# Kernel optimization log

Hardware: AMD Instinct MI355X
Metric: run time of the kernel (lower is better)

## Reference

```python
import jax, jax.numpy as jnp
import numpy as np
from jax import lax

B, IN_CH, SKIP_CH, EMBED, H, W = 4, 256, 64, 64, 64, 64
RED = 8
QC = IN_CH // RED          # 32 q/k/v channels
GUIDE = 16.0
LN_EPS = 1e-5


def conv2d(x, w, b=None, groups=1):
    # x: [B,C,H,W], w: [O, C//groups, kh, kw], SAME padding, stride 1
    y = lax.conv_general_dilated(x, w, (1, 1), 'SAME',
                                 dimension_numbers=('NCHW', 'OIHW', 'NCHW'),
                                 feature_group_count=groups)
    return y if b is None else y + b[None, :, None, None]


def deform_conv(x, off, w, b):
    # torchvision DeformConv2d (DCNv1), 3x3, stride 1, pad 1
    # x: [B,C,H,W], off: [B,18,H,W] with (dy,dx) interleaved per kernel tap
    Bx, C, Hh, Ww = x.shape
    K = 9
    off = off.reshape(Bx, K, 2, Hh, Ww)
    gy, gx = jnp.meshgrid(jnp.arange(Hh, dtype=x.dtype),
                          jnp.arange(Ww, dtype=x.dtype), indexing='ij')
    kdy, kdx = jnp.meshgrid(jnp.arange(3, dtype=x.dtype) - 1,
                            jnp.arange(3, dtype=x.dtype) - 1, indexing='ij')
    py = gy[None, None] + kdy.reshape(K)[None, :, None, None] + off[:, :, 0]  # [B,K,H,W]
    px = gx[None, None] + kdx.reshape(K)[None, :, None, None] + off[:, :, 1]
    y0f = jnp.floor(py); x0f = jnp.floor(px)
    wy = py - y0f; wx = px - x0f
    y0 = y0f.astype(jnp.int32); x0 = x0f.astype(jnp.int32)

    def corner(yi, xi, wgt):
        valid = ((yi >= 0) & (yi < Hh) & (xi >= 0) & (xi < Ww)).astype(x.dtype)
        yc = jnp.clip(yi, 0, Hh - 1); xc = jnp.clip(xi, 0, Ww - 1)
        # per-batch gather -> [B, C, K, H, W]
        g = jax.vmap(lambda img, yy, xx: img[:, yy, xx])(x, yc, xc)
        return g * (wgt * valid)[:, None]

    vals = (corner(y0, x0, (1 - wy) * (1 - wx)) +
            corner(y0, x0 + 1, (1 - wy) * wx) +
            corner(y0 + 1, x0, wy * (1 - wx)) +
            corner(y0 + 1, x0 + 1, wy * wx))
    O = w.shape[0]
    return jnp.einsum('bckhw,ock->bohw', vals, w.reshape(O, C, K)) + b[None, :, None, None]


def setup_inputs() -> dict:
    key = jax.random.key(0)
    ks = jax.random.split(key, 16)
    rn = lambda k, s, sc=0.05: jax.random.normal(k, s, jnp.float32) * sc
    return {
        'x': jax.random.normal(ks[0], (B, IN_CH, H, W), jnp.float32),
        'skip': jax.random.normal(ks[1], (B, SKIP_CH, H // 2, W // 2), jnp.float32),
        'qkv_w': rn(ks[2], (3 * QC, IN_CH, 1, 1)), 'qkv_b': jnp.zeros((3 * QC,), jnp.float32),
        'proj_w': rn(ks[3], (IN_CH, QC, 1, 1)), 'proj_b': jnp.zeros((IN_CH,), jnp.float32),
        'edge_w': rn(ks[4], (SKIP_CH, 1, 3, 3)),
        'thick_w': rn(ks[5], (1, SKIP_CH, 1, 1)), 'thick_b': jnp.zeros((1,), jnp.float32),
        'off_w': rn(ks[6], (18, SKIP_CH, 3, 3), 0.02), 'off_b': jnp.zeros((18,), jnp.float32),
        'deform_w': rn(ks[7], (SKIP_CH, SKIP_CH, 3, 3)), 'deform_b': jnp.zeros((SKIP_CH,), jnp.float32),
        'ln_g': jnp.ones((EMBED,), jnp.float32), 'ln_b': jnp.zeros((EMBED,), jnp.float32),
        'mlp1_w': rn(ks[8], (4 * EMBED, EMBED, 1, 1)), 'mlp1_b': jnp.zeros((4 * EMBED,), jnp.float32),
        'dw_w': rn(ks[9], (4 * EMBED, 1, 3, 3)), 'dw_b': jnp.zeros((4 * EMBED,), jnp.float32),
        'mlp2_w': rn(ks[10], (EMBED, 4 * EMBED, 1, 1)), 'mlp2_b': jnp.zeros((EMBED,), jnp.float32),
        'down_w': rn(ks[11], (EMBED, IN_CH + SKIP_CH, 1, 1)), 'down_b': jnp.zeros((EMBED,), jnp.float32),
        'up_w': rn(ks[12], (IN_CH, EMBED, 1, 1)), 'up_b': jnp.zeros((IN_CH,), jnp.float32),
    }


def reference(x, skip, qkv_w, qkv_b, proj_w, proj_b, edge_w, thick_w, thick_b,
              off_w, off_b, deform_w, deform_b, ln_g, ln_b,
              mlp1_w, mlp1_b, dw_w, dw_b, mlp2_w, mlp2_b,
              down_w, down_b, up_w, up_b):
    Bx, C, Hh, Ww = x.shape
    # bilinear upsample (align_corners=False == half-pixel)
    skip_u = jax.image.resize(skip, (Bx, skip.shape[1], Hh, Ww), method='bilinear')

    # ---- EfficientCrossModalAttention ----
    qkv = conv2d(x, qkv_w, qkv_b)
    q, k, v = jnp.split(qkv, 3, axis=1)           # each [B, QC, H, W]
    c = q.shape[1]
    qf = q.reshape(Bx, c, Hh * Ww).transpose(0, 2, 1)   # [B, N, c]
    kf = k.reshape(Bx, c, Hh * Ww)                       # [B, c, N]
    vf = v.reshape(Bx, c, Hh * Ww).transpose(0, 2, 1)   # [B, N, c]
    attn = jax.nn.softmax(jnp.einsum('bnc,bcm->bnm', qf, kf) / jnp.sqrt(jnp.float32(c)), axis=-1)
    av = jnp.einsum('bnm,bmc->bnc', attn, vf).transpose(0, 2, 1).reshape(Bx, c, Hh, Ww)
    x2 = conv2d(av, proj_w, proj_b) + x

    # ---- edge / offset / deformable conv ----
    edge = conv2d(skip_u.mean(1, keepdims=True), edge_w)          # no bias
    thick = jax.nn.sigmoid(conv2d(skip_u, thick_w, thick_b))
    off = conv2d(edge, off_w, off_b) * (1.0 + GUIDE * thick)
    d = deform_conv(skip_u, off, deform_w, deform_b) + edge

    # ---- down -> TokenMixerBlock -> up ----
    e = conv2d(jnp.concatenate([x2, d], axis=1), down_w, down_b)  # [B, EMBED, H, W]
    h = e.transpose(0, 2, 3, 1)
    mu = h.mean(-1, keepdims=True)
    var = ((h - mu) ** 2).mean(-1, keepdims=True)
    h = (h - mu) / jnp.sqrt(var + LN_EPS) * ln_g + ln_b
    h = h.transpose(0, 3, 1, 2)
    h = jax.nn.gelu(conv2d(h, mlp1_w, mlp1_b), approximate=False)
    h = jax.nn.gelu(conv2d(h, dw_w, dw_b, groups=4 * EMBED), approximate=False)
    h = conv2d(h, mlp2_w, mlp2_b)
    t = h + e
    return conv2d(t, up_w, up_b)
```

## Files before the change

kernel.cpp:

```cpp
#include <hip/hip_runtime.h>
#include <hip/hip_bf16.h>
#include <math.h>

#define NB 4
#define NHW 4096
#define NBN (NB * NHW)

typedef const float* fp;
typedef unsigned short us;
typedef __attribute__((ext_vector_type(8))) short short8;
typedef __attribute__((ext_vector_type(4))) float floatx4;

__device__ __forceinline__ float b2f(__hip_bfloat16 v) { return __bfloat162float(v); }
__device__ __forceinline__ __hip_bfloat16 f2b(float v) { return __float2bfloat16(v); }
__device__ __forceinline__ us f2bu(float f) {
  __hip_bfloat16 h = __float2bfloat16(f);
  return *reinterpret_cast<us*>(&h);
}
__device__ __forceinline__ float bu2f(us u) {
  __hip_bfloat16 h = *reinterpret_cast<__hip_bfloat16*>(&u);
  return __bfloat162float(h);
}
__device__ __forceinline__ float gelu_ex(float x) { return 0.5f * x * (1.0f + erff(x * 0.70710678118654752f)); }
__device__ __forceinline__ short8 ld8(const us* p) { return *(const short8*)p; }

__global__ __launch_bounds__(256) void k_wq(fp qw, us* wq) {
  int i = blockIdx.x * 256 + threadIdx.x;
  if (i >= 96 * 256) return;
  wq[i] = f2bu(qw[i]);
}

__global__ __launch_bounds__(256) void k_wcast(fp pw, fp m1w, fp dnw, fp m2w, fp uw, fp dww,
                                               fp ew, fp ow, us* wc) {
  int i = blockIdx.x * 256 + threadIdx.x;
  if (i >= 99136) return;
  float v;
  if (i < 8192) v = pw[i];
  else if (i < 24576) v = m1w[i - 8192];
  else if (i < 45056) v = dnw[i - 24576];
  else if (i < 61440) v = m2w[i - 45056];
  else if (i < 77824) v = uw[i - 61440];
  else if (i < 80128) {
    int i2 = i - 77824;
    v = dww[(i2 & 255) * 9 + (i2 >> 8)];
  } else if (i < 80704) {
    int i2 = i - 80128;
    v = ew[(i2 & 63) * 9 + (i2 >> 6)];
  } else {
    int i2 = i - 80704;
    int oc = i2 / 576, rem = i2 % 576;
    int tap = rem >> 6, c = rem & 63;
    v = (oc < 18) ? ow[(oc * 64 + c) * 9 + tap] : 0.f;
  }
  wc[i] = f2bu(v);
}

__global__ __launch_bounds__(256) void k_wprep(fp dw, us* wbf) {
  int idx = blockIdx.x * 256 + threadIdx.x;
  if (idx >= 9 * 64 * 64) return;
  int c = idx & 63, oc = (idx >> 6) & 63, k = idx >> 12;
  wbf[idx] = f2bu(dw[(oc * 64 + c) * 9 + k]);
}

__global__ __launch_bounds__(256) void k_upsample(fp skip, float* su) {
  int idx = blockIdx.x * 256 + threadIdx.x;
  if (idx >= NB * 64 * NHW) return;
  int hw = idx & 4095, bc = idx >> 12;
  int y = hw >> 6, x = hw & 63;
  float fy = 0.5f * y - 0.25f, fx = 0.5f * x - 0.25f;
  float y0f = floorf(fy), x0f = floorf(fx);
  float wy = fy - y0f, wx = fx - x0f;
  int y0 = (int)y0f, x0 = (int)x0f;
  int y0c = min(31, max(0, y0)), y1c = min(31, max(0, y0 + 1));
  int x0c = min(31, max(0, x0)), x1c = min(31, max(0, x0 + 1));
  const float* p = skip + (size_t)bc * 1024;
  float v00 = p[y0c * 32 + x0c], v01 = p[y0c * 32 + x1c];
  float v10 = p[y1c * 32 + x0c], v11 = p[y1c * 32 + x1c];
  su[idx] = (1.f - wy) * ((1.f - wx) * v00 + wx * v01) + wy * ((1.f - wx) * v10 + wx * v11);
}

__global__ __launch_bounds__(256) void k_xpose(fp x, us* xT) {
  __shared__ float tile[64][65];
  int bid = blockIdx.x;
  int pt = bid & 63, ct = (bid >> 6) & 3, b = bid >> 8;
  int px0 = pt * 64, c0 = ct * 64;
  int tx = threadIdx.x & 63, ty = threadIdx.x >> 6;
  const float* src = x + ((size_t)(b * 256 + c0)) * NHW + px0;
#pragma unroll
  for (int i = 0; i < 16; i++) {
    int r = i * 4 + ty;
    tile[r][tx] = src[(size_t)r * NHW + tx];
  }
  __syncthreads();
  int cseg = threadIdx.x & 7, p0 = threadIdx.x >> 3;
#pragma unroll
  for (int h = 0; h < 2; h++) {
    int p = p0 + h * 32;
    short8 v;
#pragma unroll
    for (int j = 0; j < 8; j++) v[j] = (short)f2bu(tile[cseg * 8 + j][p]);
    *(short8*)&xT[((size_t)(b * NHW) + px0 + p) * 256 + c0 + cseg * 8] = v;
  }
}

__global__ __launch_bounds__(256) void k_qkv_g(const us* xT, const us* wq, fp bias, us* qkvb) {
  int wave = threadIdx.x >> 6, lane = threadIdx.x & 63;
  int quad = lane >> 4, l16 = lane & 15;
  int pxg0 = blockIdx.x * 64 + wave * 16;
  int b = pxg0 >> 12, hw0 = pxg0 & 4095;
  floatx4 acc[6];
#pragma unroll
  for (int m = 0; m < 6; m++) acc[m] = (floatx4){0.f, 0.f, 0.f, 0.f};
  const us* xrow = xT + (size_t)(pxg0 + l16) * 256 + quad * 8;
#pragma unroll
  for (int k0 = 0; k0 < 256; k0 += 32) {
    short8 bf = ld8(xrow + k0);
#pragma unroll
    for (int m = 0; m < 6; m++) {
      short8 af = ld8(wq + (size_t)(m * 16 + l16) * 256 + k0 + quad * 8);
      acc[m] = __builtin_amdgcn_mfma_f32_16x16x32_bf16(af, bf, acc[m], 0, 0, 0);
    }
  }
#pragma unroll
  for (int m = 0; m < 6; m++)
#pragma unroll
    for (int r = 0; r < 4; r++) {
      int oc = m * 16 + quad * 4 + r;
      float v = acc[m][r] + bias[oc];
      if (oc < 32) v *= 0.17677669529663688f;
      qkvb[(size_t)(b * 96 + oc) * NHW + hw0 + l16] = f2bu(v);
    }
}

__global__ __launch_bounds__(256) void k_attn(const us* qkvb, us* Opart, float* ml) {
  __shared__ __align__(16) us kt[128 * 40];
  __shared__ __align__(16) us vt[32 * 136];
  __shared__ __align__(16) us pt[4][16 * 136];
  int tid = threadIdx.x;
  int wave = tid >> 6, lane = tid & 63;
  int quad = lane >> 4, l16 = lane & 15;
  int blk = blockIdx.x;
  int kh = blk & 3;
  int rest = blk >> 2;
  int b = rest >> 6;
  int qbase = (rest & 63) * 64 + wave * 16;
  const us* qp = qkvb + (size_t)b * 96 * NHW;
  const us* kp = qp + 32 * NHW;
  const us* vp = qp + 64 * NHW;

  short8 aq;
#pragma unroll
  for (int j = 0; j < 8; j++)
    aq[j] = (short)qp[(size_t)(quad * 8 + j) * NHW + qbase + l16];

  float m_r[4], l_r[4];
  floatx4 o0 = {0.f, 0.f, 0.f, 0.f}, o1 = {0.f, 0.f, 0.f, 0.f};
#pragma unroll
  for (int r = 0; r < 4; r++) { m_r[r] = -1e30f; l_r[r] = 0.f; }

  int sc = tid & 31, sg = tid >> 5;
  int vc = tid >> 3, vs = tid & 7;

  int kb0 = kh * 1024;
  for (int kb = kb0; kb < kb0 + 1024; kb += 128) {
    __syncthreads();
    {
      const us* src = kp + (size_t)sc * NHW + kb + sg * 16;
#pragma unroll
      for (int j = 0; j < 16; j++) kt[(sg * 16 + j) * 40 + sc] = src[j];
      const us* sv = vp + (size_t)vc * NHW + kb + vs * 16;
      uint4 d0 = *(const uint4*)sv;
      uint4 d1 = *(const uint4*)(sv + 8);
      *(uint4*)&vt[vc * 136 + vs * 16] = d0;
      *(uint4*)&vt[vc * 136 + vs * 16 + 8] = d1;
    }
    __syncthreads();

    floatx4 s[8];
#pragma unroll
    for (int t = 0; t < 8; t++) {
      short8 bk = *(const short8*)&kt[(t * 16 + l16) * 40 + quad * 8];
      floatx4 z = {0.f, 0.f, 0.f, 0.f};
      s[t] = __builtin_amdgcn_mfma_f32_16x16x32_bf16(aq, bk, z, 0, 0, 0);
    }

    float mnew[4], alpha[4];
#pragma unroll
    for (int r = 0; r < 4; r++) {
      float mx = s[0][r];
#pragma unroll
      for (int t = 1; t < 8; t++) mx = fmaxf(mx, s[t][r]);
#pragma unroll
      for (int msk = 1; msk < 16; msk <<= 1) mx = fmaxf(mx, __shfl_xor(mx, msk, 64));
      mnew[r] = fmaxf(m_r[r], mx);
      alpha[r] = __expf(m_r[r] - mnew[r]);
      m_r[r] = mnew[r];
    }
    float rs[4] = {0.f, 0.f, 0.f, 0.f};
#pragma unroll
    for (int t = 0; t < 8; t++) {
#pragma unroll
      for (int r = 0; r < 4; r++) {
        float p = __expf(s[t][r] - mnew[r]);
        rs[r] += p;
        pt[wave][(quad * 4 + r) * 136 + t * 16 + l16] = f2bu(p);
      }
    }
#pragma unroll
    for (int r = 0; r < 4; r++) {
      float sm = rs[r];
#pragma unroll
      for (int msk = 1; msk < 16; msk <<= 1) sm += __shfl_xor(sm, msk, 64);
      l_r[r] = l_r[r] * alpha[r] + sm;
      o0[r] *= alpha[r];
      o1[r] *= alpha[r];
    }

#pragma unroll
    for (int t = 0; t < 4; t++) {
      short8 ap  = *(const short8*)&pt[wave][l16 * 136 + t * 32 + quad * 8];
      short8 bv0 = *(const short8*)&vt[l16 * 136 + t * 32 + quad * 8];
      short8 bv1 = *(const short8*)&vt[(l16 + 16) * 136 + t * 32 + quad * 8];
      o0 = __builtin_amdgcn_mfma_f32_16x16x32_bf16(ap, bv0, o0, 0, 0, 0);
      o1 = __builtin_amdgcn_mfma_f32_16x16x32_bf16(ap, bv1, o1, 0, 0, 0);
    }
  }

#pragma unroll
  for (int r = 0; r < 4; r++) {
    int q = qbase + quad * 4 + r;
    int qg = b * NHW + q;
    us* dst = Opart + ((size_t)(kh * NBN) + qg) * 32;
    dst[l16] = f2bu(o0[r]);
    dst[l16 + 16] = f2bu(o1[r]);
    if (l16 == 0) {
      ml[kh * NBN + qg] = m_r[r];
      ml[4 * NBN + kh * NBN + qg] = l_r[r];
    }
  }
}

__global__ __launch_bounds__(256) void k_merge(const us* Opart, const float* ml, us* avb) {
  int idx = blockIdx.x * 256 + threadIdx.x;
  int ch = idx & 31, qg = idx >> 5;
  float mk[4];
  float m = -1e30f;
#pragma unroll
  for (int kh = 0; kh < 4; kh++) { mk[kh] = ml[kh * NBN + qg]; m = fmaxf(m, mk[kh]); }
  float l = 0.f, v = 0.f;
#pragma unroll
  for (int kh = 0; kh < 4; kh++) {
    float a = __expf(mk[kh] - m);
    l += ml[4 * NBN + kh * NBN + qg] * a;
    v += bu2f(Opart[((size_t)(kh * NBN) + qg) * 32 + ch]) * a;
  }
  avb[idx] = f2bu(v / l);
}

__global__ __launch_bounds__(256) void k_proj_g(const us* avb, const us* xT, const us* wpj, fp bias, us* x2T) {
  int wave = threadIdx.x >> 6, lane = threadIdx.x & 63;
  int quad = lane >> 4, l16 = lane & 15;
  int pxg0 = blockIdx.x * 64 + wave * 16;
  short8 act = ld8(avb + (size_t)(pxg0 + l16) * 32 + quad * 8);
  floatx4 acc[16];
#pragma unroll
  for (int n = 0; n < 16; n++) {
    short8 wf = ld8(wpj + (size_t)(n * 16 + l16) * 32 + quad * 8);
    floatx4 z = {0.f, 0.f, 0.f, 0.f};
    acc[n] = __builtin_amdgcn_mfma_f32_16x16x32_bf16(act, wf, z, 0, 0, 0);
  }
#pragma unroll
  for (int n = 0; n < 16; n++)
#pragma unroll
    for (int r = 0; r < 4; r++) {
      int px = pxg0 + quad * 4 + r;
      int oc = n * 16 + l16;
      size_t oidx = (size_t)px * 256 + oc;
      x2T[oidx] = f2bu(acc[n][r] + bias[oc] + bu2f(xT[oidx]));
    }
}

__global__ __launch_bounds__(256) void k_meanthick(const float* su, fp tw, fp tb, float* sm, float* thick) {
  int idx = blockIdx.x * 256 + threadIdx.x;
  if (idx >= NB * NHW) return;
  int hw = idx & 4095, b = idx >> 12;
  const float* p = su + (size_t)b * 64 * NHW + hw;
  float s = 0.f, ts = 0.f;
#pragma unroll 8
  for (int c = 0; c < 64; c++) {
    float v = p[(size_t)c * NHW];
    s += v;
    ts += v * tw[c];
  }
  sm[idx] = s * (1.f / 64.f);
  float z = ts + tb[0];
  thick[idx] = 1.f / (1.f + __expf(-z));
}

__global__ __launch_bounds__(256) void k_edge_px(const float* sm, const us* ewT, us* edgeT) {
  int idx = blockIdx.x * 256 + threadIdx.x;
  int cb = idx & 7, pxg = idx >> 3;
  int b = pxg >> 12, hw = pxg & 4095;
  int y = hw >> 6, x = hw & 63;
  int c0 = cb * 8;
  float acc[8] = {0.f, 0.f, 0.f, 0.f, 0.f, 0.f, 0.f, 0.f};
#pragma unroll
  for (int ky = 0; ky < 3; ky++) {
#pragma unroll
    for (int kx = 0; kx < 3; kx++) {
      int yy = y + ky - 1, xx = x + kx - 1;
      if (yy >= 0 && yy < 64 && xx >= 0 && xx < 64) {
        float sv = sm[b * NHW + yy * 64 + xx];
        short8 wv = ld8(ewT + (ky * 3 + kx) * 64 + c0);
#pragma unroll
        for (int j = 0; j < 8; j++) acc[j] += sv * bu2f((us)wv[j]);
      }
    }
  }
  short8 pk;
#pragma unroll
  for (int j = 0; j < 8; j++) pk[j] = (short)f2bu(acc[j]);
  *(short8*)(edgeT + (size_t)pxg * 64 + c0) = pk;
}

__global__ __launch_bounds__(256) void k_off_g(const us* edgeT, const us* woff, fp ob,
                                               const float* thick, float* offb) {
  int wave = threadIdx.x >> 6, lane = threadIdx.x & 63;
  int quad = lane >> 4, l16 = lane & 15;
  int pxg0 = blockIdx.x * 64 + wave * 16;
  int b = pxg0 >> 12;
  int pxl = pxg0 + l16;
  int hwl = pxl & 4095;
  int yl = hwl >> 6, xl = hwl & 63;
  floatx4 acc[2];
  acc[0] = (floatx4){0.f, 0.f, 0.f, 0.f};
  acc[1] = (floatx4){0.f, 0.f, 0.f, 0.f};
  const short8 zz = {0, 0, 0, 0, 0, 0, 0, 0};
#pragma unroll
  for (int t = 0; t < 9; t++) {
    int yy = yl + t / 3 - 1, xx = xl + t % 3 - 1;
    bool valid = (yy >= 0 && yy < 64 && xx >= 0 && xx < 64);
    const us* arow = edgeT + ((size_t)(b * NHW + yy * 64 + xx)) * 64;
#pragma unroll
    for (int s = 0; s < 2; s++) {
      short8 act = valid ? ld8(arow + s * 32 + quad * 8) : zz;
      int kk = t * 64 + s * 32 + quad * 8;
#pragma unroll
      for (int n = 0; n < 2; n++) {
        short8 wf = ld8(woff + (size_t)(n * 16 + l16) * 576 + kk);
        acc[n] = __builtin_amdgcn_mfma_f32_16x16x32_bf16(act, wf, acc[n], 0, 0, 0);
      }
    }
  }
#pragma unroll
  for (int n = 0; n < 2; n++)
#pragma unroll
    for (int r = 0; r < 4; r++) {
      int oc = n * 16 + l16;
      if (oc < 18) {
        int px = pxg0 + quad * 4 + r;
        int hw = px & 4095;
        float v = (acc[n][r] + ob[oc]) * (1.f + 16.f * thick[px]);
        offb[(size_t)(b * 18 + oc) * NHW + hw] = v;
      }
    }
}

__global__ __launch_bounds__(256) void k_deform(const float* su, const float* offb,
                                                const us* wbf, fp db,
                                                const us* edgeT, us* dbufT) {
  __shared__ __align__(16) us samT[4][16][72];
  int tid = threadIdx.x;
  int wave = tid >> 6, lane = tid & 63;
  int quad = lane >> 4, l16 = lane & 15;
  int b = blockIdx.x >> 6, row = blockIdx.x & 63;
  const float* sub = su + (size_t)b * 64 * NHW;

  int sp = lane & 15, sq = lane >> 4;
  int hw_s = row * 64 + wave * 16 + sp;
  int x_s = wave * 16 + sp;

  floatx4 acc[4];
#pragma unroll
  for (int a = 0; a < 4; a++) acc[a] = (floatx4){0.f, 0.f, 0.f, 0.f};

  for (int k = 0; k < 9; k++) {
    float dy = offb[((size_t)(b * 18 + 2 * k)) * NHW + hw_s];
    float dx = offb[((size_t)(b * 18 + 2 * k + 1)) * NHW + hw_s];
    float py = (float)(row + k / 3 - 1) + dy;
    float pxf = (float)(x_s + k % 3 - 1) + dx;
    float y0f = floorf(py), x0f = floorf(pxf);
    float wy = py - y0f, wx = pxf - x0f;
    int y0 = (int)y0f, x0 = (int)x0f;
    int y1 = y0 + 1, x1 = x0 + 1;
    float vy0 = (y0 >= 0 && y0 < 64) ? 1.f : 0.f;
    float vy1 = (y1 >= 0 && y1 < 64) ? 1.f : 0.f;
    float vx0 = (x0 >= 0 && x0 < 64) ? 1.f : 0.f;
    float vx1 = (x1 >= 0 && x1 < 64) ? 1.f : 0.f;
    float w00 = (1.f - wy) * (1.f - wx) * vy0 * vx0;
    float w01 = (1.f - wy) * wx * vy0 * vx1;
    float w10 = wy * (1.f - wx) * vy1 * vx0;
    float w11 = wy * wx * vy1 * vx1;
    int y0c = min(63, max(0, y0)), y1c = min(63, max(0, y1));
    int x0c = min(63, max(0, x0)), x1c = min(63, max(0, x1));
    int i00 = y0c * 64 + x0c, i01 = y0c * 64 + x1c;
    int i10 = y1c * 64 + x0c, i11 = y1c * 64 + x1c;

#pragma unroll
    for (int i = 0; i < 16; i += 2) {
      int c0 = sq * 16 + i;
      const float* s0 = sub + (size_t)c0 * NHW;
      const float* s1 = s0 + NHW;
      float v0 = w00 * s0[i00] + w01 * s0[i01] + w10 * s0[i10] + w11 * s0[i11];
      float v1 = w00 * s1[i00] + w01 * s1[i01] + w10 * s1[i10] + w11 * s1[i11];
      unsigned int pk = (unsigned int)f2bu(v0) | ((unsigned int)f2bu(v1) << 16);
      *(unsigned int*)&samT[wave][sp][c0] = pk;
    }

#pragma unroll
    for (int s = 0; s < 2; s++) {
      short8 bfrag = *(const short8*)&samT[wave][l16][s * 32 + quad * 8];
#pragma unroll
      for (int a = 0; a < 4; a++) {
        short8 afrag = ld8(wbf + ((size_t)(k * 64 + a * 16 + l16) * 64 + s * 32 + quad * 8));
        acc[a] = __builtin_amdgcn_mfma_f32_16x16x32_bf16(bfrag, afrag, acc[a], 0, 0, 0);
      }
    }
  }

#pragma unroll
  for (int a = 0; a < 4; a++)
#pragma unroll
    for (int r = 0; r < 4; r++) {
      int oc = a * 16 + l16;
      int pxr = row * 64 + wave * 16 + quad * 4 + r;
      size_t rowi = (size_t)(b * NHW) + pxr;
      float v = acc[a][r] + db[oc] + bu2f(edgeT[rowi * 64 + oc]);
      dbufT[rowi * 64 + oc] = f2bu(v);
    }
}

__global__ __launch_bounds__(256) void k_down_g(const us* x2T, const us* dbufT, const us* wd, fp bias, float* ebufT) {
  int wave = threadIdx.x >> 6, lane = threadIdx.x & 63;
  int quad = lane >> 4, l16 = lane & 15;
  int pxg0 = blockIdx.x * 64 + wave * 16;
  floatx4 acc[4];
#pragma unroll
  for (int m = 0; m < 4; m++) acc[m] = (floatx4){0.f, 0.f, 0.f, 0.f};
  const us* xrow = x2T + (size_t)(pxg0 + l16) * 256 + quad * 8;
#pragma unroll
  for (int k0 = 0; k0 < 256; k0 += 32) {
    short8 act = ld8(xrow + k0);
#pragma unroll
    for (int m = 0; m < 4; m++) {
      short8 wf = ld8(wd + (size_t)(m * 16 + l16) * 320 + k0 + quad * 8);
      acc[m] = __builtin_amdgcn_mfma_f32_16x16x32_bf16(act, wf, acc[m], 0, 0, 0);
    }
  }
  const us* drow = dbufT + (size_t)(pxg0 + l16) * 64 + quad * 8;
#pragma unroll
  for (int k0 = 0; k0 < 64; k0 += 32) {
    short8 act = ld8(drow + k0);
#pragma unroll
    for (int m = 0; m < 4; m++) {
      short8 wf = ld8(wd + (size_t)(m * 16 + l16) * 320 + 256 + k0 + quad * 8);
      acc[m] = __builtin_amdgcn_mfma_f32_16x16x32_bf16(act, wf, acc[m], 0, 0, 0);
    }
  }
#pragma unroll
  for (int m = 0; m < 4; m++)
#pragma unroll
    for (int r = 0; r < 4; r++) {
      int px = pxg0 + quad * 4 + r;
      int oc = m * 16 + l16;
      ebufT[(size_t)px * 64 + oc] = acc[m][r] + bias[oc];
    }
}

__global__ __launch_bounds__(256) void k_ln(const float* eT, fp g, fp bt, us* hnT) {
  int idx = blockIdx.x * 256 + threadIdx.x;
  if (idx >= NB * NHW) return;
  const float* p = eT + (size_t)idx * 64;
  float v[64];
  float s = 0.f;
#pragma unroll
  for (int i = 0; i < 16; i++) {
    float4 t = ((const float4*)p)[i];
    v[i * 4] = t.x; v[i * 4 + 1] = t.y; v[i * 4 + 2] = t.z; v[i * 4 + 3] = t.w;
    s += t.x + t.y + t.z + t.w;
  }
  float mu = s * (1.f / 64.f);
  float q = 0.f;
#pragma unroll
  for (int c = 0; c < 64; c++) { float d = v[c] - mu; q += d * d; }
  float rstd = rsqrtf(q * (1.f / 64.f) + 1e-5f);
  us* o = hnT + (size_t)idx * 64;
#pragma unroll
  for (int j = 0; j < 8; j++) {
    short8 pk;
#pragma unroll
    for (int t = 0; t < 8; t++) {
      int c = j * 8 + t;
      pk[t] = (short)f2bu((v[c] - mu) * rstd * g[c] + bt[c]);
    }
    *(short8*)(o + j * 8) = pk;
  }
}

__global__ __launch_bounds__(256) void k_mlp1_g(const us* hnT, const us* wm1, fp bias, us* h1T) {
  int wave = threadIdx.x >> 6, lane = threadIdx.x & 63;
  int quad = lane >> 4, l16 = lane & 15;
  int pxg0 = blockIdx.x * 64 + wave * 16;
  floatx4 acc[16];
#pragma unroll
  for (int m = 0; m < 16; m++) acc[m] = (floatx4){0.f, 0.f, 0.f, 0.f};
  const us* hrow = hnT + (size_t)(pxg0 + l16) * 64 + quad * 8;
#pragma unroll
  for (int k0 = 0; k0 < 64; k0 += 32) {
    short8 act = ld8(hrow + k0);
#pragma unroll
    for (int m = 0; m < 16; m++) {
      short8 wf = ld8(wm1 + (size_t)(m * 16 + l16) * 64 + k0 + quad * 8);
      acc[m] = __builtin_amdgcn_mfma_f32_16x16x32_bf16(act, wf, acc[m], 0, 0, 0);
    }
  }
#pragma unroll
  for (int m = 0; m < 16; m++)
#pragma unroll
    for (int r = 0; r < 4; r++) {
      int px = pxg0 + quad * 4 + r;
      int oc = m * 16 + l16;
      h1T[(size_t)px * 256 + oc] = f2bu(gelu_ex(acc[m][r] + bias[oc]));
    }
}

__global__ __launch_bounds__(256) void k_dw(const us* h1T, const us* wdwT, fp bias, us* h2T) {
  int idx = blockIdx.x * 256 + threadIdx.x;
  int cb = idx & 31, pxg = idx >> 5;
  int b = pxg >> 12, hw = pxg & 4095;
  int y = hw >> 6, x = hw & 63;
  int c0 = cb * 8;
  float4 b0 = *(const float4*)(bias + c0);
  float4 b1 = *(const float4*)(bias + c0 + 4);
  float acc[8] = {b0.x, b0.y, b0.z, b0.w, b1.x, b1.y, b1.z, b1.w};
#pragma unroll
  for (int ky = 0; ky < 3; ky++) {
#pragma unroll
    for (int kx = 0; kx < 3; kx++) {
      int tap = ky * 3 + kx;
      short8 wv = ld8(wdwT + tap * 256 + c0);
      int yy = y + ky - 1, xx = x + kx - 1;
      if (yy >= 0 && yy < 64 && xx >= 0 && xx < 64) {
        short8 vv = ld8(h1T + ((size_t)(b * NHW + yy * 64 + xx)) * 256 + c0);
#pragma unroll
        for (int j = 0; j < 8; j++)
          acc[j] += bu2f((us)vv[j]) * bu2f((us)wv[j]);
      }
    }
  }
  short8 pk;
#pragma unroll
  for (int j = 0; j < 8; j++) pk[j] = (short)f2bu(gelu_ex(acc[j]));
  *(short8*)(h2T + (size_t)pxg * 256 + c0) = pk;
}

__global__ __launch_bounds__(256) void k_mlp2_g(const us* h2T, const us* wm2, fp bias, const float* ebufT, us* tbufT) {
  int wave = threadIdx.x >> 6, lane = threadIdx.x & 63;
  int quad = lane >> 4, l16 = lane & 15;
  int pxg0 = blockIdx.x * 64 + wave * 16;
  floatx4 acc[4];
#pragma unroll
  for (int m = 0; m < 4; m++) acc[m] = (floatx4){0.f, 0.f, 0.f, 0.f};
  const us* hrow = h2T + (size_t)(pxg0 + l16) * 256 + quad * 8;
#pragma unroll
  for (int k0 = 0; k0 < 256; k0 += 32) {
    short8 act = ld8(hrow + k0);
#pragma unroll
    for (int m = 0; m < 4; m++) {
      short8 wf = ld8(wm2 + (size_t)(m * 16 + l16) * 256 + k0 + quad * 8);
      acc[m] = __builtin_amdgcn_mfma_f32_16x16x32_bf16(act, wf, acc[m], 0, 0, 0);
    }
  }
#pragma unroll
  for (int m = 0; m < 4; m++)
#pragma unroll
    for (int r = 0; r < 4; r++) {
      int px = pxg0 + quad * 4 + r;
      int oc = m * 16 + l16;
      size_t oidx = (size_t)px * 64 + oc;
      tbufT[oidx] = f2bu(acc[m][r] + bias[oc] + ebufT[oidx]);
    }
}

__global__ __launch_bounds__(256) void k_up_g(const us* tbufT, const us* wu, fp bias, float* out) {
  int wave = threadIdx.x >> 6, lane = threadIdx.x & 63;
  int quad = lane >> 4, l16 = lane & 15;
  int pxg0 = blockIdx.x * 64 + wave * 16;
  int b = pxg0 >> 12, hw0 = pxg0 & 4095;
  floatx4 acc[16];
#pragma unroll
  for (int m = 0; m < 16; m++) acc[m] = (floatx4){0.f, 0.f, 0.f, 0.f};
  const us* trow = tbufT + (size_t)(pxg0 + l16) * 64 + quad * 8;
#pragma unroll
  for (int k0 = 0; k0 < 64; k0 += 32) {
    short8 bf = ld8(trow + k0);
#pragma unroll
    for (int m = 0; m < 16; m++) {
      short8 af = ld8(wu + (size_t)(m * 16 + l16) * 64 + k0 + quad * 8);
      acc[m] = __builtin_amdgcn_mfma_f32_16x16x32_bf16(af, bf, acc[m], 0, 0, 0);
    }
  }
#pragma unroll
  for (int m = 0; m < 16; m++)
#pragma unroll
    for (int r = 0; r < 4; r++) {
      int oc = m * 16 + quad * 4 + r;
      out[(size_t)(b * 256 + oc) * NHW + hw0 + l16] = acc[m][r] + bias[oc];
    }
}

extern "C" void kernel_launch(void* const* d_in, const int* in_sizes, int n_in,
                              void* d_out, int out_size, void* d_ws, size_t ws_size,
                              hipStream_t stream) {
  fp x = (fp)d_in[0], skip = (fp)d_in[1], qkv_w = (fp)d_in[2], qkv_b = (fp)d_in[3],
     proj_w = (fp)d_in[4], proj_b = (fp)d_in[5], edge_w = (fp)d_in[6], thick_w = (fp)d_in[7],
     thick_b = (fp)d_in[8], off_w = (fp)d_in[9], off_b = (fp)d_in[10], deform_w = (fp)d_in[11],
     deform_b = (fp)d_in[12], ln_g = (fp)d_in[13], ln_b = (fp)d_in[14], mlp1_w = (fp)d_in[15],
     mlp1_b = (fp)d_in[16], dw_w = (fp)d_in[17], dw_b = (fp)d_in[18], mlp2_w = (fp)d_in[19],
     mlp2_b = (fp)d_in[20], down_w = (fp)d_in[21], down_b = (fp)d_in[22], up_w = (fp)d_in[23],
     up_b = (fp)d_in[24];

  float* ws = (float*)d_ws;
  float* su    = ws + 0;
  us* qkvb  = (us*)(ws + 1048576);
  us* avb   = (us*)(ws + 1835008);
  us* wc    = (us*)(ws + 2097152);
  float* ml = ws + 2146720;
  us* x2T   = (us*)(ws + 3145728);
  us* edgeT = (us*)(ws + 5242880);
  float* offb  = ws + 6291456;
  float* sm    = ws + 6586368;
  float* thick = ws + 6602752;
  us* dbufT = (us*)(ws + 6619136);
  float* ebufT = ws + 7143424;
  us* xT   = x2T;
  us* wq   = dbufT;
  us* wbf  = (us*)sm;
  us* Opart = (us*)ebufT;
  us* hnT  = qkvb;
  us* h1T  = x2T;
  us* h2T  = (us*)ws;
  us* tbufT = edgeT;

  dim3 blk(256);
  k_wq<<<96, blk, 0, stream>>>(qkv_w, wq);
  k_wcast<<<388, blk, 0, stream>>>(proj_w, mlp1_w, down_w, mlp2_w, up_w, dw_w, edge_w, off_w, wc);
  k_upsample<<<(NB * 64 * NHW) / 256, blk, 0, stream>>>(skip, su);
  k_xpose<<<1024, blk, 0, stream>>>(x, xT);
  k_qkv_g<<<(NB * NHW) / 64, blk, 0, stream>>>(xT, wq, qkv_b, qkvb);
  k_attn<<<(NB * NHW) / 16, blk, 0, stream>>>(qkvb, Opart, ml);
  k_merge<<<(NB * NHW * 32) / 256, blk, 0, stream>>>(Opart, ml, avb);
  k_proj_g<<<(NB * NHW) / 64, blk, 0, stream>>>(avb, xT, wc, proj_b, x2T);
  k_meanthick<<<(NB * NHW) / 256, blk, 0, stream>>>(su, thick_w, thick_b, sm, thick);
  k_edge_px<<<(NB * NHW * 8) / 256, blk, 0, stream>>>(sm, wc + 80128, edgeT);
  k_off_g<<<(NB * NHW) / 64, blk, 0, stream>>>(edgeT, wc + 80704, off_b, thick, offb);
  k_wprep<<<144, blk, 0, stream>>>(deform_w, wbf);
  k_deform<<<NB * 64, blk, 0, stream>>>(su, offb, wbf, deform_b, edgeT, dbufT);
  k_down_g<<<(NB * NHW) / 64, blk, 0, stream>>>(x2T, dbufT, wc + 24576, down_b, ebufT);
  k_ln<<<(NB * NHW) / 256, blk, 0, stream>>>(ebufT, ln_g, ln_b, hnT);
  k_mlp1_g<<<(NB * NHW) / 64, blk, 0, stream>>>(hnT, wc + 8192, mlp1_b, h1T);
  k_dw<<<(NB * NHW * 32) / 256, blk, 0, stream>>>(h1T, wc + 77824, dw_b, h2T);
  k_mlp2_g<<<(NB * NHW) / 64, blk, 0, stream>>>(h2T, wc + 45056, mlp2_b, ebufT, tbufT);
  k_up_g<<<(NB * NHW) / 64, blk, 0, stream>>>(tbufT, wc + 61440, up_b, (float*)d_out);
}
```

Measured before the change: 308.0 us.

## Restructure flash attention: pixel-major K, transposed scores, register P via permlane swaps

The QKV kernel now writes K pixel-major into a separate buffer, so the attention kernel can load K fragments straight from global memory into registers and prefetch the next block. It drops the shared-memory staging and both barriers. Scores are computed transposed (K·Q), which leaves one query per lane, so the softmax needs only two cross-lane shuffles. The Q scale is folded into log2e so exp2f replaces __expf. P is rearranged in registers with permlane32/16 swaps instead of a shared-memory round trip, V is read directly from global memory, and s_setprio and a launch bound of 4 blocks are added. The risks are uncached global V reads and heavier register pressure.

```diff
diff --git a/kernel.cpp b/kernel.cpp
--- a/kernel.cpp
+++ b/kernel.cpp
@@ -9,7 +9,10 @@
 typedef const float* fp;
 typedef unsigned short us;
 typedef __attribute__((ext_vector_type(8))) short short8;
+typedef __attribute__((ext_vector_type(4))) short short4v;
 typedef __attribute__((ext_vector_type(4))) float floatx4;
+typedef __attribute__((ext_vector_type(2))) unsigned int uint2v;
+typedef __attribute__((ext_vector_type(4))) unsigned int uint4v;
 
 __device__ __forceinline__ float b2f(__hip_bfloat16 v) { return __bfloat162float(v); }
 __device__ __forceinline__ __hip_bfloat16 f2b(float v) { return __float2bfloat16(v); }
@@ -103,7 +106,7 @@
   }
 }
 
-__global__ __launch_bounds__(256) void k_qkv_g(const us* xT, const us* wq, fp bias, us* qkvb) {
+__global__ __launch_bounds__(256) void k_qkv_g(const us* xT, const us* wq, fp bias, us* qkvb, us* kpx) {
   int wave = threadIdx.x >> 6, lane = threadIdx.x & 63;
   int quad = lane >> 4, l16 = lane & 15;
   int pxg0 = blockIdx.x * 64 + wave * 16;
@@ -122,20 +125,28 @@
     }
   }
 #pragma unroll
-  for (int m = 0; m < 6; m++)
-#pragma unroll
-    for (int r = 0; r < 4; r++) {
-      int oc = m * 16 + quad * 4 + r;
-      float v = acc[m][r] + bias[oc];
-      if (oc < 32) v *= 0.17677669529663688f;
-      qkvb[(size_t)(b * 96 + oc) * NHW + hw0 + l16] = f2bu(v);
-    }
-}
-
-__global__ __launch_bounds__(256) void k_attn(const us* qkvb, us* Opart, float* ml) {
-  __shared__ __align__(16) us kt[128 * 40];
-  __shared__ __align__(16) us vt[32 * 136];
-  __shared__ __align__(16) us pt[4][16 * 136];
+  for (int m = 0; m < 6; m++) {
+    if (m == 2 || m == 3) {
+      short4v pkv;
+#pragma unroll
+      for (int r = 0; r < 4; r++) {
+        int oc = m * 16 + quad * 4 + r;
+        pkv[r] = (short)f2bu(acc[m][r] + bias[oc]);
+      }
+      *(short4v*)&kpx[((size_t)(b * NHW) + hw0 + l16) * 32 + (m - 2) * 16 + quad * 4] = pkv;
+    } else {
+#pragma unroll
+      for (int r = 0; r < 4; r++) {
+        int oc = m * 16 + quad * 4 + r;
+        float v = acc[m][r] + bias[oc];
+        if (oc < 32) v *= 0.25503485f;
+        qkvb[(size_t)(b * 96 + oc) * NHW + hw0 + l16] = f2bu(v);
+      }
+    }
+  }
+}
+
+__global__ __launch_bounds__(256, 4) void k_attn(const us* qkvb, const us* kpx, us* Opart, float* ml) {
   int tid = threadIdx.x;
   int wave = tid >> 6, lane = tid & 63;
   int quad = lane >> 4, l16 = lane & 15;
@@ -145,98 +156,94 @@
   int b = rest >> 6;
   int qbase = (rest & 63) * 64 + wave * 16;
   const us* qp = qkvb + (size_t)b * 96 * NHW;
-  const us* kp = qp + 32 * NHW;
   const us* vp = qp + 64 * NHW;
-
-  short8 aq;
+  const us* kb_base = kpx + (size_t)b * NHW * 32;
+
+  short8 bq;
 #pragma unroll
   for (int j = 0; j < 8; j++)
-    aq[j] = (short)qp[(size_t)(quad * 8 + j) * NHW + qbase + l16];
-
-  float m_r[4], l_r[4];
+    bq[j] = (short)qp[(size_t)(quad * 8 + j) * NHW + qbase + l16];
+
+  float m_r = -1e30f, l_r = 0.f;
   floatx4 o0 = {0.f, 0.f, 0.f, 0.f}, o1 = {0.f, 0.f, 0.f, 0.f};
-#pragma unroll
-  for (int r = 0; r < 4; r++) { m_r[r] = -1e30f; l_r[r] = 0.f; }
-
-  int sc = tid & 31, sg = tid >> 5;
-  int vc = tid >> 3, vs = tid & 7;
 
   int kb0 = kh * 1024;
+  short8 akf[8];
+#pragma unroll
+  for (int t = 0; t < 8; t++)
+    akf[t] = ld8(kb_base + (size_t)(kb0 + t * 16 + l16) * 32 + quad * 8);
+
   for (int kb = kb0; kb < kb0 + 1024; kb += 128) {
-    __syncthreads();
-    {
-      const us* src = kp + (size_t)sc * NHW + kb + sg * 16;
-#pragma unroll
-      for (int j = 0; j < 16; j++) kt[(sg * 16 + j) * 40 + sc] = src[j];
-      const us* sv = vp + (size_t)vc * NHW + kb + vs * 16;
-      uint4 d0 = *(const uint4*)sv;
-      uint4 d1 = *(const uint4*)(sv + 8);
-      *(uint4*)&vt[vc * 136 + vs * 16] = d0;
-      *(uint4*)&vt[vc * 136 + vs * 16 + 8] = d1;
-    }
-    __syncthreads();
-
-    floatx4 s[8];
+    floatx4 sT[8];
+    __builtin_amdgcn_s_setprio(1);
 #pragma unroll
     for (int t = 0; t < 8; t++) {
-      short8 bk = *(const short8*)&kt[(t * 16 + l16) * 40 + quad * 8];
       floatx4 z = {0.f, 0.f, 0.f, 0.f};
-      s[t] = __builtin_amdgcn_mfma_f32_16x16x32_bf16(aq, bk, z, 0, 0, 0);
-    }
-
-    float mnew[4], alpha[4];
-#pragma unroll
-    for (int r = 0; r < 4; r++) {
-      float mx = s[0][r];
-#pragma unroll
-      for (int t = 1; t < 8; t++) mx = fmaxf(mx, s[t][r]);
-#pragma unroll
-      for (int msk = 1; msk < 16; msk <<= 1) mx = fmaxf(mx, __shfl_xor(mx, msk, 64));
-      mnew[r] = fmaxf(m_r[r], mx);
-      alpha[r] = __expf(m_r[r] - mnew[r]);
-      m_r[r] = mnew[r];
-    }
-    float rs[4] = {0.f, 0.f, 0.f, 0.f};
+      sT[t] = __builtin_amdgcn_mfma_f32_16x16x32_bf16(akf[t], bq, z, 0, 0, 0);
+    }
+    __builtin_amdgcn_s_setprio(0);
+
+    int kbn = (kb + 128 < kb0 + 1024) ? kb + 128 : kb0;
+#pragma unroll
+    for (int t = 0; t < 8; t++)
+      akf[t] = ld8(kb_base + (size_t)(kbn + t * 16 + l16) * 32 + quad * 8);
+
+    float mx = fmaxf(fmaxf(sT[0][0], sT[0][1]), fmaxf(sT[0][2], sT[0][3]));
+#pragma unroll
+    for (int t = 1; t < 8; t++)
+      mx = fmaxf(mx, fmaxf(fmaxf(sT[t][0], sT[t][1]), fmaxf(sT[t][2], sT[t][3])));
+    mx = fmaxf(mx, __shfl_xor(mx, 16));
+    mx = fmaxf(mx, __shfl_xor(mx, 32));
+    float mnew = fmaxf(m_r, mx);
+    float alpha = exp2f(m_r - mnew);
+    m_r = mnew;
+
+    float rs = 0.f;
+    unsigned pkw[8][2];
 #pragma unroll
     for (int t = 0; t < 8; t++) {
-#pragma unroll
-      for (int r = 0; r < 4; r++) {
-        float p = __expf(s[t][r] - mnew[r]);
-        rs[r] += p;
-        pt[wave][(quad * 4 + r) * 136 + t * 16 + l16] = f2bu(p);
-      }
-    }
-#pragma unroll
-    for (int r = 0; r < 4; r++) {
-      float sm = rs[r];
-#pragma unroll
-      for (int msk = 1; msk < 16; msk <<= 1) sm += __shfl_xor(sm, msk, 64);
-      l_r[r] = l_r[r] * alpha[r] + sm;
-      o0[r] *= alpha[r];
-      o1[r] *= alpha[r];
-    }
-
-#pragma unroll
-    for (int t = 0; t < 4; t++) {
-      short8 ap  = *(const short8*)&pt[wave][l16 * 136 + t * 32 + quad * 8];
-      short8 bv0 = *(const short8*)&vt[l16 * 136 + t * 32 + quad * 8];
-      short8 bv1 = *(const short8*)&vt[(l16 + 16) * 136 + t * 32 + quad * 8];
-      o0 = __builtin_amdgcn_mfma_f32_16x16x32_bf16(ap, bv0, o0, 0, 0, 0);
-      o1 = __builtin_amdgcn_mfma_f32_16x16x32_bf16(ap, bv1, o1, 0, 0, 0);
-    }
-  }
-
-#pragma unroll
-  for (int r = 0; r < 4; r++) {
-    int q = qbase + quad * 4 + r;
-    int qg = b * NHW + q;
-    us* dst = Opart + ((size_t)(kh * NBN) + qg) * 32;
-    dst[l16] = f2bu(o0[r]);
-    dst[l16 + 16] = f2bu(o1[r]);
-    if (l16 == 0) {
-      ml[kh * NBN + qg] = m_r[r];
-      ml[4 * NBN + kh * NBN + qg] = l_r[r];
-    }
+      float p0 = exp2f(sT[t][0] - mnew);
+      float p1 = exp2f(sT[t][1] - mnew);
+      float p2 = exp2f(sT[t][2] - mnew);
+      float p3 = exp2f(sT[t][3] - mnew);
+      rs += (p0 + p1) + (p2 + p3);
+      pkw[t][0] = (unsigned)f2bu(p0) | ((unsigned)f2bu(p1) << 16);
+      pkw[t][1] = (unsigned)f2bu(p2) | ((unsigned)f2bu(p3) << 16);
+    }
+    rs += __shfl_xor(rs, 16);
+    rs += __shfl_xor(rs, 32);
+    l_r = l_r * alpha + rs;
+#pragma unroll
+    for (int r = 0; r < 4; r++) { o0[r] *= alpha; o1[r] *= alpha; }
+
+    __builtin_amdgcn_s_setprio(1);
+#pragma unroll
+    for (int cc = 0; cc < 4; cc++) {
+      uint2v t1 = __builtin_amdgcn_permlane32_swap(pkw[2 * cc][0], pkw[2 * cc + 1][0], false, false);
+      uint2v t2 = __builtin_amdgcn_permlane16_swap(t1.x, t1.y, false, false);
+      uint2v t3 = __builtin_amdgcn_permlane32_swap(pkw[2 * cc][1], pkw[2 * cc + 1][1], false, false);
+      uint2v t4 = __builtin_amdgcn_permlane16_swap(t3.x, t3.y, false, false);
+      uint4v pw = {t2.x, t4.x, t2.y, t4.y};
+      short8 pa = *(short8*)&pw;
+      short8 av0 = ld8(vp + (size_t)l16 * NHW + kb + cc * 32 + quad * 8);
+      short8 av1 = ld8(vp + (size_t)(l16 + 16) * NHW + kb + cc * 32 + quad * 8);
+      o0 = __builtin_amdgcn_mfma_f32_16x16x32_bf16(av0, pa, o0, 0, 0, 0);
+      o1 = __builtin_amdgcn_mfma_f32_16x16x32_bf16(av1, pa, o1, 0, 0, 0);
+    }
+    __builtin_amdgcn_s_setprio(0);
+  }
+
+  int q = qbase + l16;
+  size_t qg = (size_t)b * NHW + q;
+  us* dst = Opart + ((size_t)kh * NBN + qg) * 32;
+  short4v e0, e1;
+#pragma unroll
+  for (int r = 0; r < 4; r++) { e0[r] = (short)f2bu(o0[r]); e1[r] = (short)f2bu(o1[r]); }
+  *(short4v*)(dst + quad * 4) = e0;
+  *(short4v*)(dst + 16 + quad * 4) = e1;
+  if (quad == 0) {
+    ml[(size_t)kh * NBN + qg] = m_r;
+    ml[(size_t)4 * NBN + (size_t)kh * NBN + qg] = l_r;
   }
 }
 
@@ -250,7 +257,7 @@
   float l = 0.f, v = 0.f;
 #pragma unroll
   for (int kh = 0; kh < 4; kh++) {
-    float a = __expf(mk[kh] - m);
+    float a = exp2f(mk[kh] - m);
     l += ml[4 * NBN + kh * NBN + qg] * a;
     v += bu2f(Opart[((size_t)(kh * NBN) + qg) * 32 + ch]) * a;
   }
@@ -636,6 +643,7 @@
   us* avb   = (us*)(ws + 1835008);
   us* wc    = (us*)(ws + 2097152);
   float* ml = ws + 2146720;
+  us* kpx   = (us*)(ws + 2277792);
   us* x2T   = (us*)(ws + 3145728);
   us* edgeT = (us*)(ws + 5242880);
   float* offb  = ws + 6291456;
@@ -657,8 +665,8 @@
   k_wcast<<<388, blk, 0, stream>>>(proj_w, mlp1_w, down_w, mlp2_w, up_w, dw_w, edge_w, off_w, wc);
   k_upsample<<<(NB * 64 * NHW) / 256, blk, 0, stream>>>(skip, su);
   k_xpose<<<1024, blk, 0, stream>>>(x, xT);
-  k_qkv_g<<<(NB * NHW) / 64, blk, 0, stream>>>(xT, wq, qkv_b, qkvb);
-  k_attn<<<(NB * NHW) / 16, blk, 0, stream>>>(qkvb, Opart, ml);
+  k_qkv_g<<<(NB * NHW) / 64, blk, 0, stream>>>(xT, wq, qkv_b, qkvb, kpx);
+  k_attn<<<(NB * NHW) / 16, blk, 0, stream>>>(qkvb, kpx, Opart, ml);
   k_merge<<<(NB * NHW * 32) / 256, blk, 0, stream>>>(Opart, ml, avb);
   k_proj_g<<<(NB * NHW) / 64, blk, 0, stream>>>(avb, xT, wc, proj_b, x2T);
   k_meanthick<<<(NB * NHW) / 256, blk, 0, stream>>>(su, thick_w, thick_b, sm, thick);
```

Result: slower. 316.6 us (+2.8%).
